# Performance work log

Measured on AMD Instinct MI355X. Metric: run time of the kernel, lower is better.

## Reference

```python
import jax, jax.numpy as jnp
import numpy as np
import math

B, T, D = 4, 8192, 1024
EPS = 1e-5

def setup_inputs() -> dict:
    key = jax.random.key(0)
    ks = jax.random.split(key, 8)
    xavier = lambda k, shape: jax.random.uniform(k, shape, jnp.float32,
                                                 -math.sqrt(6.0 / (shape[0] + shape[1])),
                                                 math.sqrt(6.0 / (shape[0] + shape[1])))
    x = jax.random.normal(ks[0], (B, T, D), jnp.float32)
    ln_gamma = jnp.ones((D,), jnp.float32)
    ln_beta = jnp.zeros((D,), jnp.float32)
    Wg = xavier(ks[1], (D, D))            # torch Linear weight: (out, in)
    bg = jnp.zeros((D,), jnp.float32)
    Wv = 0.01 * xavier(ks[2], (D, D))     # gain=0.01
    bv = jnp.zeros((D,), jnp.float32)
    Wo = 0.01 * xavier(ks[3], (D, D))     # gain=0.01
    bo = jnp.zeros((D,), jnp.float32)
    log_decay = jnp.asarray(math.log(math.exp(0.01) - 1.0), jnp.float32)
    return {"x": x, "ln_gamma": ln_gamma, "ln_beta": ln_beta,
            "Wg": Wg, "bg": bg, "Wv": Wv, "bv": bv, "Wo": Wo, "bo": bo,
            "log_decay": log_decay}

def reference(x, ln_gamma, ln_beta, Wg, bg, Wv, bv, Wo, bo, log_decay):
    # LayerNorm
    mu = jnp.mean(x, axis=-1, keepdims=True)
    var = jnp.mean(jnp.square(x - mu), axis=-1, keepdims=True)
    normed = (x - mu) * jax.lax.rsqrt(var + EPS) * ln_gamma + ln_beta
    # gate / value projections (torch Linear: y = x @ W.T + b)
    g = jax.nn.sigmoid(jnp.einsum('btd,ed->bte', normed, Wg) + bg)
    v = jnp.einsum('btd,ed->bte', normed, Wv) + bv
    # push-pull cumulative sums over time
    cumsum = jnp.cumsum(g * v, axis=1) - jnp.cumsum((1.0 - g) * v, axis=1)
    # positional exponential decay
    alpha = jax.nn.softplus(log_decay)
    positions = jnp.arange(x.shape[1], dtype=jnp.float32)
    decay = jnp.exp(-alpha * positions)[None, :, None]  # (1,T,1)
    out = jnp.einsum('btd,ed->bte', cumsum * decay, Wo) + bo
    return x + out  # dropout is identity at eval
```

## Files before the change

kernel.cpp:

```cpp
#include <hip/hip_runtime.h>
#include <cstdint>
#include <cstddef>

#define DD 1024
#define TT 8192
#define BB 4
#define MM (BB*TT)
#define NCHUNK 64
#define CLEN 128
#define EPS 1e-5f
#define NIT 8

typedef __attribute__((ext_vector_type(8))) short bf16x8;
typedef __attribute__((ext_vector_type(4))) float f32x4;

__device__ __forceinline__ float bf2f(unsigned short b) {
  union { unsigned int u; float f; } c; c.u = ((unsigned int)b) << 16; return c.f;
}
__device__ __forceinline__ unsigned short f2bf(float f) {
  union { float f; unsigned int u; } c; c.f = f;
  unsigned int lsb = (c.u >> 16) & 1u;
  c.u += 0x7fffu + lsb;
  return (unsigned short)(c.u >> 16);
}

__device__ __forceinline__ void gload16(const void* gsrc, void* ldst) {
  __builtin_amdgcn_global_load_lds(
      (const __attribute__((address_space(1))) unsigned int*)gsrc,
      (__attribute__((address_space(3))) unsigned int*)ldst, 16, 0, 0);
}

#define MFMA16(a, b, c) __builtin_amdgcn_mfma_f32_16x16x32_bf16((a), (b), (c), 0, 0, 0)
#define BAR    __builtin_amdgcn_s_barrier()
#define PRIO1  __builtin_amdgcn_s_setprio(1)
#define PRIO0  __builtin_amdgcn_s_setprio(0)
#define VMW(N) asm volatile("s_waitcnt vmcnt(" #N ")" ::: "memory")

__device__ __forceinline__ bf16x8 LD(const char* p, int imm) {
  return *(const bf16x8*)(p + imm);
}

__global__ __launch_bounds__(256) void cast_weights(
    const float* __restrict__ wg, const float* __restrict__ wv,
    const float* __restrict__ wo,
    unsigned short* __restrict__ owg, unsigned short* __restrict__ owv,
    unsigned short* __restrict__ owo) {
  int i = blockIdx.x * 256 + threadIdx.x;
  const float* src; unsigned short* dst; int off;
  if (i < 262144)       { src = wg; dst = owg; off = i; }
  else if (i < 524288)  { src = wv; dst = owv; off = i - 262144; }
  else                  { src = wo; dst = owo; off = i - 524288; }
  float4 v = ((const float4*)src)[off];
  ushort4 o;
  o.x = f2bf(v.x); o.y = f2bf(v.y); o.z = f2bf(v.z); o.w = f2bf(v.w);
  ((ushort4*)dst)[off] = o;
}

__global__ __launch_bounds__(256) void ln_kernel(
    const float* __restrict__ x, const float* __restrict__ gamma,
    const float* __restrict__ beta, unsigned short* __restrict__ normed) {
  size_t row = blockIdx.x;
  int tid = threadIdx.x, lane = tid & 63, wid = tid >> 6;
  float4 v = ((const float4*)(x + row * DD))[tid];
  float s = v.x + v.y + v.z + v.w;
  float q = v.x * v.x + v.y * v.y + v.z * v.z + v.w * v.w;
#pragma unroll
  for (int off = 32; off; off >>= 1) {
    s += __shfl_down(s, off);
    q += __shfl_down(q, off);
  }
  __shared__ float rs[4], rq[4];
  if (lane == 0) { rs[wid] = s; rq[wid] = q; }
  __syncthreads();
  float ts = rs[0] + rs[1] + rs[2] + rs[3];
  float tq = rq[0] + rq[1] + rq[2] + rq[3];
  float mu  = ts * (1.0f / DD);
  float var = tq * (1.0f / DD) - mu * mu;
  float rstd = rsqrtf(var + EPS);
  float4 gm = ((const float4*)gamma)[tid];
  float4 bt = ((const float4*)beta)[tid];
  ushort4 o;
  o.x = f2bf((v.x - mu) * rstd * gm.x + bt.x);
  o.y = f2bf((v.y - mu) * rstd * gm.y + bt.y);
  o.z = f2bf((v.z - mu) * rstd * gm.z + bt.z);
  o.w = f2bf((v.w - mu) * rstd * gm.w + bt.w);
  ((ushort4*)normed)[row * (DD / 4) + tid] = o;
}

__global__ __launch_bounds__(512, 2) void gemm_gv(
    const unsigned short* __restrict__ normed,
    const unsigned short* __restrict__ wg, const unsigned short* __restrict__ wv,
    const float* __restrict__ bg, const float* __restrict__ bv,
    unsigned short* __restrict__ u, float* __restrict__ sums) {
  __shared__ unsigned short As[2][2][128 * 64];
  __shared__ unsigned short Bgs[2][128 * 64];
  __shared__ unsigned short Bvs[2][128 * 64];
  int tid = threadIdx.x, lane = tid & 63, wid = tid >> 6;
  int wm = wid >> 2, wn = wid & 3;
  int swz = (blockIdx.x & 7) * (gridDim.x >> 3) + (blockIdx.x >> 3);
  int bx = swz >> 3, by = swz & 7;
  size_t m0 = (size_t)bx * 256;
  int n0 = by * 128;

  int ua = tid, ub = tid + 512;
  int ra = ua >> 3, sa = (ua & 7) ^ (ra & 7);
  int rb = ub >> 3, sb = (ub & 7) ^ (rb & 7);
  const unsigned short* gA = normed + m0 * DD;
  const unsigned short* gBg = wg + (size_t)n0 * DD;
  const unsigned short* gBv = wv + (size_t)n0 * DD;
  const unsigned short* pAa = gA + (size_t)ra * DD + sa * 8;
  const unsigned short* pAb = gA + (size_t)rb * DD + sb * 8;
  const unsigned short* pGa = gBg + (size_t)ra * DD + sa * 8;
  const unsigned short* pGb = gBg + (size_t)rb * DD + sb * 8;
  const unsigned short* pVa = gBv + (size_t)ra * DD + sa * 8;
  const unsigned short* pVb = gBv + (size_t)rb * DD + sb * 8;
  auto SA = [&](int t, int h) {
    char* d = (char*)&As[t & 1][h][0];
    gload16(pAa + (size_t)h * 128 * DD + t * 64, d + ua * 16);
    gload16(pAb + (size_t)h * 128 * DD + t * 64, d + ub * 16);
  };
  auto SG = [&](int t) {
    char* d = (char*)&Bgs[t & 1][0];
    gload16(pGa + t * 64, d + ua * 16);
    gload16(pGb + t * 64, d + ub * 16);
  };
  auto SV = [&](int t) {
    char* d = (char*)&Bvs[t & 1][0];
    gload16(pVa + t * 64, d + ua * 16);
    gload16(pVb + t * 64, d + ub * 16);
  };

  f32x4 accg[8][2], accv[8][2];
#pragma unroll
  for (int a = 0; a < 8; ++a)
#pragma unroll
    for (int b = 0; b < 2; ++b) {
      accg[a][b] = (f32x4){0.f, 0.f, 0.f, 0.f};
      accv[a][b] = (f32x4){0.f, 0.f, 0.f, 0.f};
    }

  SG(0); SV(0); SA(0, 0); SA(0, 1); SG(1); SV(1); SA(1, 0);
  VMW(6);
  BAR;

  int r = lane & 15, q = lane >> 4, rx = r & 7;
  const char* pA[2][2];
  const char* pBgL[2][2];
  const char* pBvL[2][2];
#pragma unroll
  for (int d = 0; d < 2; ++d) {
#pragma unroll
    for (int kk = 0; kk < 2; ++kk) {
      int s8 = kk * 4 + q;
      int xo = (s8 ^ rx) << 4;
      pA[d][kk]   = (const char*)&As[d][wm][0] + r * 128 + xo;
      pBgL[d][kk] = (const char*)&Bgs[d][0] + (wn * 32 + r) * 128 + xo;
      pBvL[d][kk] = (const char*)&Bvs[d][0] + (wn * 32 + r) * 128 + xo;
    }
  }

  bf16x8 am[4][2], bgf[2][2], bvf[2][2];
  for (int T = 0; T < NIT; ++T) {
    bool more = (T < NIT - 1);
    int t1 = 2 * T + 1, t2 = 2 * T + 2, t3 = 2 * T + 3;
#pragma unroll
    for (int mi = 0; mi < 4; ++mi)
#pragma unroll
      for (int kk = 0; kk < 2; ++kk)
        am[mi][kk] = LD(pA[0][kk], mi * 2048);
#pragma unroll
    for (int ni = 0; ni < 2; ++ni)
#pragma unroll
      for (int kk = 0; kk < 2; ++kk)
        bgf[ni][kk] = LD(pBgL[0][kk], ni * 2048);
    SA(t1, 1);
    BAR; PRIO1;
#pragma unroll
    for (int mi = 0; mi < 4; ++mi)
#pragma unroll
      for (int ni = 0; ni < 2; ++ni)
#pragma unroll
        for (int kk = 0; kk < 2; ++kk)
          accg[mi][ni] = MFMA16(am[mi][kk], bgf[ni][kk], accg[mi][ni]);
    PRIO0; BAR;
#pragma unroll
    for (int ni = 0; ni < 2; ++ni)
#pragma unroll
      for (int kk = 0; kk < 2; ++kk)
        bvf[ni][kk] = LD(pBvL[0][kk], ni * 2048);
    if (more) SG(t2);
    BAR; PRIO1;
#pragma unroll
    for (int mi = 0; mi < 4; ++mi)
#pragma unroll
      for (int ni = 0; ni < 2; ++ni)
#pragma unroll
        for (int kk = 0; kk < 2; ++kk)
          accv[mi][ni] = MFMA16(am[mi][kk], bvf[ni][kk], accv[mi][ni]);
    PRIO0; BAR;
#pragma unroll
    for (int mi = 0; mi < 4; ++mi)
#pragma unroll
      for (int kk = 0; kk < 2; ++kk)
        am[mi][kk] = LD(pA[0][kk], 8192 + mi * 2048);
    if (more) SV(t2);
    BAR; PRIO1;
#pragma unroll
    for (int mi = 0; mi < 4; ++mi)
#pragma unroll
      for (int ni = 0; ni < 2; ++ni)
#pragma unroll
        for (int kk = 0; kk < 2; ++kk)
          accv[4 + mi][ni] = MFMA16(am[mi][kk], bvf[ni][kk], accv[4 + mi][ni]);
    PRIO0; BAR;
    if (more) { SA(t2, 0); VMW(6); } else { VMW(0); }
    BAR; PRIO1;
#pragma unroll
    for (int mi = 0; mi < 4; ++mi)
#pragma unroll
      for (int ni = 0; ni < 2; ++ni)
#pragma unroll
        for (int kk = 0; kk < 2; ++kk)
          accg[4 + mi][ni] = MFMA16(am[mi][kk], bgf[ni][kk], accg[4 + mi][ni]);
    PRIO0; BAR;
#pragma unroll
    for (int mi = 0; mi < 4; ++mi)
#pragma unroll
      for (int kk = 0; kk < 2; ++kk)
        am[mi][kk] = LD(pA[1][kk], mi * 2048);
#pragma unroll
    for (int ni = 0; ni < 2; ++ni)
#pragma unroll
      for (int kk = 0; kk < 2; ++kk)
        bgf[ni][kk] = LD(pBgL[1][kk], ni * 2048);
    if (more) SA(t2, 1);
    BAR; PRIO1;
#pragma unroll
    for (int mi = 0; mi < 4; ++mi)
#pragma unroll
      for (int ni = 0; ni < 2; ++ni)
#pragma unroll
        for (int kk = 0; kk < 2; ++kk)
          accg[mi][ni] = MFMA16(am[mi][kk], bgf[ni][kk], accg[mi][ni]);
    PRIO0; BAR;
#pragma unroll
    for (int ni = 0; ni < 2; ++ni)
#pragma unroll
      for (int kk = 0; kk < 2; ++kk)
        bvf[ni][kk] = LD(pBvL[1][kk], ni * 2048);
    if (more) SG(t3);
    BAR; PRIO1;
#pragma unroll
    for (int mi = 0; mi < 4; ++mi)
#pragma unroll
      for (int ni = 0; ni < 2; ++ni)
#pragma unroll
        for (int kk = 0; kk < 2; ++kk)
          accv[mi][ni] = MFMA16(am[mi][kk], bvf[ni][kk], accv[mi][ni]);
    PRIO0; BAR;
#pragma unroll
    for (int mi = 0; mi < 4; ++mi)
#pragma unroll
      for (int kk = 0; kk < 2; ++kk)
        am[mi][kk] = LD(pA[1][kk], 8192 + mi * 2048);
    if (more) SV(t3);
    BAR; PRIO1;
#pragma unroll
    for (int mi = 0; mi < 4; ++mi)
#pragma unroll
      for (int ni = 0; ni < 2; ++ni)
#pragma unroll
        for (int kk = 0; kk < 2; ++kk)
          accv[4 + mi][ni] = MFMA16(am[mi][kk], bvf[ni][kk], accv[4 + mi][ni]);
    PRIO0; BAR;
    if (more) { SA(t3, 0); VMW(6); } else { VMW(0); }
    BAR; PRIO1;
#pragma unroll
    for (int mi = 0; mi < 4; ++mi)
#pragma unroll
      for (int ni = 0; ni < 2; ++ni)
#pragma unroll
        for (int kk = 0; kk < 2; ++kk)
          accg[4 + mi][ni] = MFMA16(am[mi][kk], bgf[ni][kk], accg[4 + mi][ni]);
    PRIO0; BAR;
  }

  float psum[2] = {0.f, 0.f};
#pragma unroll
  for (int mi = 0; mi < 8; ++mi)
#pragma unroll
    for (int ni = 0; ni < 2; ++ni) {
      int e = n0 + wn * 32 + ni * 16 + r;
      size_t rbase = m0 + wm * 128 + mi * 16 + q * 4;
      float bgv = bg[e], bvv = bv[e];
#pragma unroll
      for (int j = 0; j < 4; ++j) {
        float gp = accg[mi][ni][j] + bgv;
        float vp = accv[mi][ni][j] + bvv;
        float sg = 1.0f / (1.0f + __expf(-gp));
        float uu = (2.0f * sg - 1.0f) * vp;
        psum[ni] += uu;
        u[(rbase + j) * DD + e] = f2bf(uu);
      }
    }
#pragma unroll
  for (int ni = 0; ni < 2; ++ni) {
    psum[ni] += __shfl_xor(psum[ni], 16);
    psum[ni] += __shfl_xor(psum[ni], 32);
  }
  if (lane < 16) {
    int b = (int)(m0 >> 13);
    int ch = (int)((m0 & 8191) >> 7) + wm;
    size_t sidx = ((size_t)(b * NCHUNK + ch)) * DD + n0 + wn * 32 + lane;
    sums[sidx]      = psum[0];
    sums[sidx + 16] = psum[1];
  }
}

__global__ __launch_bounds__(256) void scan_chunks(float* __restrict__ sums) {
  int b = blockIdx.x >> 2;
  int e = (blockIdx.x & 3) * 256 + threadIdx.x;
  float vals[NCHUNK];
#pragma unroll
  for (int c = 0; c < NCHUNK; ++c)
    vals[c] = sums[((size_t)(b * NCHUNK + c)) * DD + e];
  float carry = 0.f;
#pragma unroll
  for (int c = 0; c < NCHUNK; ++c) {
    float t = vals[c]; vals[c] = carry; carry += t;
  }
#pragma unroll
  for (int c = 0; c < NCHUNK; ++c)
    sums[((size_t)(b * NCHUNK + c)) * DD + e] = vals[c];
}

__global__ __launch_bounds__(128) void scan_final(
    unsigned short* __restrict__ u, const float* __restrict__ sums,
    const float* __restrict__ log_decay) {
  int bid = blockIdx.x;
  int half = bid & 1, chunk = (bid >> 1) & 63, b = bid >> 7;
  int e0 = half * 512 + threadIdx.x * 4;
  float alpha = log1pf(__expf(log_decay[0]));
  float dec  = __expf(-alpha * (float)(chunk * CLEN));
  float step = __expf(-alpha);
  float4 c = *(const float4*)(sums + ((size_t)(b * NCHUNK + chunk)) * DD + e0);
  size_t base = ((size_t)b * TT + (size_t)chunk * CLEN) * DD + e0;
#pragma unroll 4
  for (int i = 0; i < CLEN; ++i) {
    ushort4 w = *(const ushort4*)(u + base + (size_t)i * DD);
    c.x += bf2f(w.x); c.y += bf2f(w.y); c.z += bf2f(w.z); c.w += bf2f(w.w);
    ushort4 o;
    o.x = f2bf(c.x * dec); o.y = f2bf(c.y * dec);
    o.z = f2bf(c.z * dec); o.w = f2bf(c.w * dec);
    *(ushort4*)(u + base + (size_t)i * DD) = o;
    dec *= step;
  }
}

__global__ __launch_bounds__(512, 2) void gemm_out(
    const unsigned short* __restrict__ cmat, const unsigned short* __restrict__ wo,
    const float* __restrict__ bo, const float* __restrict__ x,
    float* __restrict__ out) {
  __shared__ unsigned short As[2][2][128 * 64];
  __shared__ unsigned short Bs[2][2][128 * 64];
  int tid = threadIdx.x, lane = tid & 63, wid = tid >> 6;
  int wm = wid >> 2, wn = wid & 3;
  int swz = (blockIdx.x & 7) * (gridDim.x >> 3) + (blockIdx.x >> 3);
  int bx = swz >> 2, by = swz & 3;
  size_t m0 = (size_t)bx * 256;
  int n0 = by * 256;
  int bh = wn >> 1, nb = wn & 1;

  int ua = tid, ub = tid + 512;
  int ra = ua >> 3, sa = (ua & 7) ^ (ra & 7);
  int rb = ub >> 3, sb = (ub & 7) ^ (rb & 7);
  const unsigned short* gA = cmat + m0 * DD;
  const unsigned short* gB = wo + (size_t)n0 * DD;
  const unsigned short* pAa = gA + (size_t)ra * DD + sa * 8;
  const unsigned short* pAb = gA + (size_t)rb * DD + sb * 8;
  const unsigned short* pBa = gB + (size_t)ra * DD + sa * 8;
  const unsigned short* pBb = gB + (size_t)rb * DD + sb * 8;
  auto SA = [&](int t, int h) {
    char* d = (char*)&As[t & 1][h][0];
    gload16(pAa + (size_t)h * 128 * DD + t * 64, d + ua * 16);
    gload16(pAb + (size_t)h * 128 * DD + t * 64, d + ub * 16);
  };
  auto SB = [&](int t, int h) {
    char* d = (char*)&Bs[t & 1][h][0];
    gload16(pBa + (size_t)h * 128 * DD + t * 64, d + ua * 16);
    gload16(pBb + (size_t)h * 128 * DD + t * 64, d + ub * 16);
  };

  f32x4 acc[8][4];
#pragma unroll
  for (int a = 0; a < 8; ++a)
#pragma unroll
    for (int b = 0; b < 4; ++b) acc[a][b] = (f32x4){0.f, 0.f, 0.f, 0.f};

  SB(0, 0); SB(0, 1); SA(0, 0); SA(0, 1); SB(1, 0); SB(1, 1);
  VMW(4);
  BAR;

  int r = lane & 15, q = lane >> 4, rx = r & 7;
  const char* pA[2][2];
  const char* pB[2][2];
#pragma unroll
  for (int d = 0; d < 2; ++d) {
#pragma unroll
    for (int kk = 0; kk < 2; ++kk) {
      int s8 = kk * 4 + q;
      int xo = (s8 ^ rx) << 4;
      pA[d][kk] = (const char*)&As[d][wm][0] + r * 128 + xo;
      pB[d][kk] = (const char*)&Bs[d][bh][0] + (nb * 64 + r) * 128 + xo;
    }
  }

  bf16x8 am[4][2], b01[2][2], b23[2][2];
  for (int T = 0; T < NIT; ++T) {
    bool more = (T < NIT - 1);
    int t1 = 2 * T + 1, t2 = 2 * T + 2, t3 = 2 * T + 3;
#pragma unroll
    for (int mi = 0; mi < 4; ++mi)
#pragma unroll
      for (int kk = 0; kk < 2; ++kk)
        am[mi][kk] = LD(pA[0][kk], mi * 2048);
#pragma unroll
    for (int ni = 0; ni < 2; ++ni)
#pragma unroll
      for (int kk = 0; kk < 2; ++kk)
        b01[ni][kk] = LD(pB[0][kk], ni * 2048);
    SA(t1, 0);
    BAR; PRIO1;
#pragma unroll
    for (int mi = 0; mi < 4; ++mi)
#pragma unroll
      for (int ni = 0; ni < 2; ++ni)
#pragma unroll
        for (int kk = 0; kk < 2; ++kk)
          acc[mi][ni] = MFMA16(am[mi][kk], b01[ni][kk], acc[mi][ni]);
    PRIO0; BAR;
#pragma unroll
    for (int ni = 0; ni < 2; ++ni)
#pragma unroll
      for (int kk = 0; kk < 2; ++kk)
        b23[ni][kk] = LD(pB[0][kk], 4096 + ni * 2048);
    SA(t1, 1);
    BAR; PRIO1;
#pragma unroll
    for (int mi = 0; mi < 4; ++mi)
#pragma unroll
      for (int ni = 0; ni < 2; ++ni)
#pragma unroll
        for (int kk = 0; kk < 2; ++kk)
          acc[mi][2 + ni] = MFMA16(am[mi][kk], b23[ni][kk], acc[mi][2 + ni]);
    PRIO0; BAR;
#pragma unroll
    for (int mi = 0; mi < 4; ++mi)
#pragma unroll
      for (int kk = 0; kk < 2; ++kk)
        am[mi][kk] = LD(pA[0][kk], 8192 + mi * 2048);
    if (more) SB(t2, 0);
    BAR; PRIO1;
#pragma unroll
    for (int mi = 0; mi < 4; ++mi)
#pragma unroll
      for (int ni = 0; ni < 2; ++ni)
#pragma unroll
        for (int kk = 0; kk < 2; ++kk)
          acc[4 + mi][2 + ni] = MFMA16(am[mi][kk], b23[ni][kk], acc[4 + mi][2 + ni]);
    PRIO0; BAR;
    if (more) { SB(t2, 1); VMW(4); } else { VMW(0); }
    BAR; PRIO1;
#pragma unroll
    for (int mi = 0; mi < 4; ++mi)
#pragma unroll
      for (int ni = 0; ni < 2; ++ni)
#pragma unroll
        for (int kk = 0; kk < 2; ++kk)
          acc[4 + mi][ni] = MFMA16(am[mi][kk], b01[ni][kk], acc[4 + mi][ni]);
    PRIO0; BAR;
#pragma unroll
    for (int mi = 0; mi < 4; ++mi)
#pragma unroll
      for (int kk = 0; kk < 2; ++kk)
        am[mi][kk] = LD(pA[1][kk], mi * 2048);
#pragma unroll
    for (int ni = 0; ni < 2; ++ni)
#pragma unroll
      for (int kk = 0; kk < 2; ++kk)
        b01[ni][kk] = LD(pB[1][kk], ni * 2048);
    if (more) SA(t2, 0);
    BAR; PRIO1;
#pragma unroll
    for (int mi = 0; mi < 4; ++mi)
#pragma unroll
      for (int ni = 0; ni < 2; ++ni)
#pragma unroll
        for (int kk = 0; kk < 2; ++kk)
          acc[mi][ni] = MFMA16(am[mi][kk], b01[ni][kk], acc[mi][ni]);
    PRIO0; BAR;
#pragma unroll
    for (int ni = 0; ni < 2; ++ni)
#pragma unroll
      for (int kk = 0; kk < 2; ++kk)
        b23[ni][kk] = LD(pB[1][kk], 4096 + ni * 2048);
    if (more) SA(t2, 1);
    BAR; PRIO1;
#pragma unroll
    for (int mi = 0; mi < 4; ++mi)
#pragma unroll
      for (int ni = 0; ni < 2; ++ni)
#pragma unroll
        for (int kk = 0; kk < 2; ++kk)
          acc[mi][2 + ni] = MFMA16(am[mi][kk], b23[ni][kk], acc[mi][2 + ni]);
    PRIO0; BAR;
#pragma unroll
    for (int mi = 0; mi < 4; ++mi)
#pragma unroll
      for (int kk = 0; kk < 2; ++kk)
        am[mi][kk] = LD(pA[1][kk], 8192 + mi * 2048);
    if (more) SB(t3, 0);
    BAR; PRIO1;
#pragma unroll
    for (int mi = 0; mi < 4; ++mi)
#pragma unroll
      for (int ni = 0; ni < 2; ++ni)
#pragma unroll
        for (int kk = 0; kk < 2; ++kk)
          acc[4 + mi][2 + ni] = MFMA16(am[mi][kk], b23[ni][kk], acc[4 + mi][2 + ni]);
    PRIO0; BAR;
    if (more) { SB(t3, 1); VMW(4); } else { VMW(0); }
    BAR; PRIO1;
#pragma unroll
    for (int mi = 0; mi < 4; ++mi)
#pragma unroll
      for (int ni = 0; ni < 2; ++ni)
#pragma unroll
        for (int kk = 0; kk < 2; ++kk)
          acc[4 + mi][ni] = MFMA16(am[mi][kk], b01[ni][kk], acc[4 + mi][ni]);
    PRIO0; BAR;
  }

#pragma unroll
  for (int mi = 0; mi < 8; ++mi)
#pragma unroll
    for (int nq = 0; nq < 4; ++nq) {
      int e = n0 + wn * 64 + nq * 16 + r;
      size_t rbase = m0 + wm * 128 + mi * 16 + q * 4;
      float bov = bo[e];
#pragma unroll
      for (int j = 0; j < 4; ++j) {
        size_t idx = (rbase + j) * DD + e;
        out[idx] = x[idx] + bov + acc[mi][nq][j];
      }
    }
}

extern "C" void kernel_launch(void* const* d_in, const int* in_sizes, int n_in,
                              void* d_out, int out_size, void* d_ws, size_t ws_size,
                              hipStream_t stream) {
  const float* x     = (const float*)d_in[0];
  const float* gamma = (const float*)d_in[1];
  const float* beta  = (const float*)d_in[2];
  const float* Wg    = (const float*)d_in[3];
  const float* bg    = (const float*)d_in[4];
  const float* Wv    = (const float*)d_in[5];
  const float* bv    = (const float*)d_in[6];
  const float* Wo    = (const float*)d_in[7];
  const float* bo    = (const float*)d_in[8];
  const float* ldcy  = (const float*)d_in[9];
  float* out = (float*)d_out;

  char* ws = (char*)d_ws;
  unsigned short* normed = (unsigned short*)ws;
  unsigned short* u      = (unsigned short*)(ws + (size_t)67108864);
  unsigned short* wgb    = (unsigned short*)(ws + (size_t)134217728);
  unsigned short* wvb    = wgb + 1048576;
  unsigned short* wob    = wvb + 1048576;
  float* sums            = (float*)(ws + (size_t)134217728 + (size_t)3 * 2097152);

  cast_weights<<<3072, 256, 0, stream>>>(Wg, Wv, Wo, wgb, wvb, wob);
  ln_kernel<<<MM, 256, 0, stream>>>(x, gamma, beta, normed);
  gemm_gv<<<dim3(MM / 256 * (DD / 128)), 512, 0, stream>>>(normed, wgb, wvb, bg, bv, u, sums);
  scan_chunks<<<BB * (DD / 256), 256, 0, stream>>>(sums);
  scan_final<<<BB * NCHUNK * 2, 128, 0, stream>>>(u, sums, ldcy);
  gemm_out<<<dim3(MM / 256 * (DD / 256)), 512, 0, stream>>>(u, wob, bo, x, out);
}
```

Before: 335.9 us.

## Interleave gate and value weights into one concatenated matrix for single GEMM

Weight casting now writes Wg and Wv rows interleaved (alternating per row) into one 2048-row bf16 matrix, so the gate/value projection runs as a single 256x256-tile GEMM over a unified B buffer rather than two separate B streams. The epilogue pairs adjacent columns with a lane shuffle to combine gate and value before computing the push-pull product and chunk sums. This simplifies the staged pipeline and uniformly loads B tiles, at the cost of half the lanes idling in the epilogue and extra shuffles.

After: 398.7 us. 1.19x slower.

```diff
diff --git a/kernel.cpp b/kernel.cpp
--- a/kernel.cpp
+++ b/kernel.cpp
@@ -43,17 +43,16 @@
 __global__ __launch_bounds__(256) void cast_weights(
     const float* __restrict__ wg, const float* __restrict__ wv,
     const float* __restrict__ wo,
-    unsigned short* __restrict__ owg, unsigned short* __restrict__ owv,
-    unsigned short* __restrict__ owo) {
+    unsigned short* __restrict__ wcat, unsigned short* __restrict__ owo) {
   int i = blockIdx.x * 256 + threadIdx.x;
-  const float* src; unsigned short* dst; int off;
-  if (i < 262144)       { src = wg; dst = owg; off = i; }
-  else if (i < 524288)  { src = wv; dst = owv; off = i - 262144; }
-  else                  { src = wo; dst = owo; off = i - 524288; }
+  const float* src; unsigned short* dst; int off, dun;
+  if (i < 262144)       { src = wg; off = i;          dst = wcat; dun = ((off & ~255) << 1) | (off & 255); }
+  else if (i < 524288)  { src = wv; off = i - 262144; dst = wcat; dun = ((off & ~255) << 1) | 256 | (off & 255); }
+  else                  { src = wo; off = i - 524288; dst = owo;  dun = off; }
   float4 v = ((const float4*)src)[off];
   ushort4 o;
   o.x = f2bf(v.x); o.y = f2bf(v.y); o.z = f2bf(v.z); o.w = f2bf(v.w);
-  ((ushort4*)dst)[off] = o;
+  ((ushort4*)dst)[dun] = o;
 }
 
 __global__ __launch_bounds__(256) void ln_kernel(
@@ -89,77 +88,64 @@
 
 __global__ __launch_bounds__(512, 2) void gemm_gv(
     const unsigned short* __restrict__ normed,
-    const unsigned short* __restrict__ wg, const unsigned short* __restrict__ wv,
+    const unsigned short* __restrict__ wcat,
     const float* __restrict__ bg, const float* __restrict__ bv,
     unsigned short* __restrict__ u, float* __restrict__ sums) {
   __shared__ unsigned short As[2][2][128 * 64];
-  __shared__ unsigned short Bgs[2][128 * 64];
-  __shared__ unsigned short Bvs[2][128 * 64];
+  __shared__ unsigned short Bs[2][2][128 * 64];
   int tid = threadIdx.x, lane = tid & 63, wid = tid >> 6;
   int wm = wid >> 2, wn = wid & 3;
   int swz = (blockIdx.x & 7) * (gridDim.x >> 3) + (blockIdx.x >> 3);
   int bx = swz >> 3, by = swz & 7;
   size_t m0 = (size_t)bx * 256;
-  int n0 = by * 128;
+  int n0 = by * 256;
+  int bh = wn >> 1, nb = wn & 1;
 
   int ua = tid, ub = tid + 512;
   int ra = ua >> 3, sa = (ua & 7) ^ (ra & 7);
   int rb = ub >> 3, sb = (ub & 7) ^ (rb & 7);
   const unsigned short* gA = normed + m0 * DD;
-  const unsigned short* gBg = wg + (size_t)n0 * DD;
-  const unsigned short* gBv = wv + (size_t)n0 * DD;
+  const unsigned short* gB = wcat + (size_t)n0 * DD;
   const unsigned short* pAa = gA + (size_t)ra * DD + sa * 8;
   const unsigned short* pAb = gA + (size_t)rb * DD + sb * 8;
-  const unsigned short* pGa = gBg + (size_t)ra * DD + sa * 8;
-  const unsigned short* pGb = gBg + (size_t)rb * DD + sb * 8;
-  const unsigned short* pVa = gBv + (size_t)ra * DD + sa * 8;
-  const unsigned short* pVb = gBv + (size_t)rb * DD + sb * 8;
+  const unsigned short* pBa = gB + (size_t)ra * DD + sa * 8;
+  const unsigned short* pBb = gB + (size_t)rb * DD + sb * 8;
   auto SA = [&](int t, int h) {
     char* d = (char*)&As[t & 1][h][0];
     gload16(pAa + (size_t)h * 128 * DD + t * 64, d + ua * 16);
     gload16(pAb + (size_t)h * 128 * DD + t * 64, d + ub * 16);
   };
-  auto SG = [&](int t) {
-    char* d = (char*)&Bgs[t & 1][0];
-    gload16(pGa + t * 64, d + ua * 16);
-    gload16(pGb + t * 64, d + ub * 16);
+  auto SB = [&](int t, int h) {
+    char* d = (char*)&Bs[t & 1][h][0];
+    gload16(pBa + (size_t)h * 128 * DD + t * 64, d + ua * 16);
+    gload16(pBb + (size_t)h * 128 * DD + t * 64, d + ub * 16);
   };
-  auto SV = [&](int t) {
-    char* d = (char*)&Bvs[t & 1][0];
-    gload16(pVa + t * 64, d + ua * 16);
-    gload16(pVb + t * 64, d + ub * 16);
-  };
-
-  f32x4 accg[8][2], accv[8][2];
+
+  f32x4 acc[8][4];
 #pragma unroll
   for (int a = 0; a < 8; ++a)
 #pragma unroll
-    for (int b = 0; b < 2; ++b) {
-      accg[a][b] = (f32x4){0.f, 0.f, 0.f, 0.f};
-      accv[a][b] = (f32x4){0.f, 0.f, 0.f, 0.f};
-    }
-
-  SG(0); SV(0); SA(0, 0); SA(0, 1); SG(1); SV(1); SA(1, 0);
-  VMW(6);
+    for (int b = 0; b < 4; ++b) acc[a][b] = (f32x4){0.f, 0.f, 0.f, 0.f};
+
+  SB(0, 0); SB(0, 1); SA(0, 0); SA(0, 1); SB(1, 0); SB(1, 1);
+  VMW(4);
   BAR;
 
   int r = lane & 15, q = lane >> 4, rx = r & 7;
   const char* pA[2][2];
-  const char* pBgL[2][2];
-  const char* pBvL[2][2];
+  const char* pB[2][2];
 #pragma unroll
   for (int d = 0; d < 2; ++d) {
 #pragma unroll
     for (int kk = 0; kk < 2; ++kk) {
       int s8 = kk * 4 + q;
       int xo = (s8 ^ rx) << 4;
-      pA[d][kk]   = (const char*)&As[d][wm][0] + r * 128 + xo;
-      pBgL[d][kk] = (const char*)&Bgs[d][0] + (wn * 32 + r) * 128 + xo;
-      pBvL[d][kk] = (const char*)&Bvs[d][0] + (wn * 32 + r) * 128 + xo;
+      pA[d][kk] = (const char*)&As[d][wm][0] + r * 128 + xo;
+      pB[d][kk] = (const char*)&Bs[d][bh][0] + (nb * 64 + r) * 128 + xo;
     }
   }
 
-  bf16x8 am[4][2], bgf[2][2], bvf[2][2];
+  bf16x8 am[4][2], b01[2][2], b23[2][2];
   for (int T = 0; T < NIT; ++T) {
     bool more = (T < NIT - 1);
     int t1 = 2 * T + 1, t2 = 2 * T + 2, t3 = 2 * T + 3;
@@ -172,7 +158,22 @@
     for (int ni = 0; ni < 2; ++ni)
 #pragma unroll
       for (int kk = 0; kk < 2; ++kk)
-        bgf[ni][kk] = LD(pBgL[0][kk], ni * 2048);
+        b01[ni][kk] = LD(pB[0][kk], ni * 2048);
+    SA(t1, 0);
+    BAR; PRIO1;
+#pragma unroll
+    for (int mi = 0; mi < 4; ++mi)
+#pragma unroll
+      for (int ni = 0; ni < 2; ++ni)
+#pragma unroll
+        for (int kk = 0; kk < 2; ++kk)
+          acc[mi][ni] = MFMA16(am[mi][kk], b01[ni][kk], acc[mi][ni]);
+    PRIO0; BAR;
+#pragma unroll
+    for (int ni = 0; ni < 2; ++ni)
+#pragma unroll
+      for (int kk = 0; kk < 2; ++kk)
+        b23[ni][kk] = LD(pB[0][kk], 4096 + ni * 2048);
     SA(t1, 1);
     BAR; PRIO1;
 #pragma unroll
@@ -181,47 +182,32 @@
       for (int ni = 0; ni < 2; ++ni)
 #pragma unroll
         for (int kk = 0; kk < 2; ++kk)
-          accg[mi][ni] = MFMA16(am[mi][kk], bgf[ni][kk], accg[mi][ni]);
-    PRIO0; BAR;
-#pragma unroll
-    for (int ni = 0; ni < 2; ++ni)
-#pragma unroll
-      for (int kk = 0; kk < 2; ++kk)
-        bvf[ni][kk] = LD(pBvL[0][kk], ni * 2048);
-    if (more) SG(t2);
-    BAR; PRIO1;
-#pragma unroll
-    for (int mi = 0; mi < 4; ++mi)
-#pragma unroll
-      for (int ni = 0; ni < 2; ++ni)
-#pragma unroll
-        for (int kk = 0; kk < 2; ++kk)
-          accv[mi][ni] = MFMA16(am[mi][kk], bvf[ni][kk], accv[mi][ni]);
+          acc[mi][2 + ni] = MFMA16(am[mi][kk], b23[ni][kk], acc[mi][2 + ni]);
     PRIO0; BAR;
 #pragma unroll
     for (int mi = 0; mi < 4; ++mi)
 #pragma unroll
       for (int kk = 0; kk < 2; ++kk)
         am[mi][kk] = LD(pA[0][kk], 8192 + mi * 2048);
-    if (more) SV(t2);
-    BAR; PRIO1;
-#pragma unroll
-    for (int mi = 0; mi < 4; ++mi)
-#pragma unroll
-      for (int ni = 0; ni < 2; ++ni)
-#pragma unroll
-        for (int kk = 0; kk < 2; ++kk)
-          accv[4 + mi][ni] = MFMA16(am[mi][kk], bvf[ni][kk], accv[4 + mi][ni]);
-    PRIO0; BAR;
-    if (more) { SA(t2, 0); VMW(6); } else { VMW(0); }
-    BAR; PRIO1;
-#pragma unroll
-    for (int mi = 0; mi < 4; ++mi)
-#pragma unroll
-      for (int ni = 0; ni < 2; ++ni)
-#pragma unroll
-        for (int kk = 0; kk < 2; ++kk)
-          accg[4 + mi][ni] = MFMA16(am[mi][kk], bgf[ni][kk], accg[4 + mi][ni]);
+    if (more) SB(t2, 0);
+    BAR; PRIO1;
+#pragma unroll
+    for (int mi = 0; mi < 4; ++mi)
+#pragma unroll
+      for (int ni = 0; ni < 2; ++ni)
+#pragma unroll
+        for (int kk = 0; kk < 2; ++kk)
+          acc[4 + mi][2 + ni] = MFMA16(am[mi][kk], b23[ni][kk], acc[4 + mi][2 + ni]);
+    PRIO0; BAR;
+    if (more) { SB(t2, 1); VMW(4); } else { VMW(0); }
+    BAR; PRIO1;
+#pragma unroll
+    for (int mi = 0; mi < 4; ++mi)
+#pragma unroll
+      for (int ni = 0; ni < 2; ++ni)
+#pragma unroll
+        for (int kk = 0; kk < 2; ++kk)
+          acc[4 + mi][ni] = MFMA16(am[mi][kk], b01[ni][kk], acc[4 + mi][ni]);
     PRIO0; BAR;
 #pragma unroll
     for (int mi = 0; mi < 4; ++mi)
@@ -232,7 +218,22 @@
     for (int ni = 0; ni < 2; ++ni)
 #pragma unroll
       for (int kk = 0; kk < 2; ++kk)
-        bgf[ni][kk] = LD(pBgL[1][kk], ni * 2048);
+        b01[ni][kk] = LD(pB[1][kk], ni * 2048);
+    if (more) SA(t2, 0);
+    BAR; PRIO1;
+#pragma unroll
+    for (int mi = 0; mi < 4; ++mi)
+#pragma unroll
+      for (int ni = 0; ni < 2; ++ni)
+#pragma unroll
+        for (int kk = 0; kk < 2; ++kk)
+          acc[mi][ni] = MFMA16(am[mi][kk], b01[ni][kk], acc[mi][ni]);
+    PRIO0; BAR;
+#pragma unroll
+    for (int ni = 0; ni < 2; ++ni)
+#pragma unroll
+      for (int kk = 0; kk < 2; ++kk)
+        b23[ni][kk] = LD(pB[1][kk], 4096 + ni * 2048);
     if (more) SA(t2, 1);
     BAR; PRIO1;
 #pragma unroll
@@ -241,79 +242,71 @@
       for (int ni = 0; ni < 2; ++ni)
 #pragma unroll
         for (int kk = 0; kk < 2; ++kk)
-          accg[mi][ni] = MFMA16(am[mi][kk], bgf[ni][kk], accg[mi][ni]);
-    PRIO0; BAR;
-#pragma unroll
-    for (int ni = 0; ni < 2; ++ni)
-#pragma unroll
-      for (int kk = 0; kk < 2; ++kk)
-        bvf[ni][kk] = LD(pBvL[1][kk], ni * 2048);
-    if (more) SG(t3);
-    BAR; PRIO1;
-#pragma unroll
-    for (int mi = 0; mi < 4; ++mi)
-#pragma unroll
-      for (int ni = 0; ni < 2; ++ni)
-#pragma unroll
-        for (int kk = 0; kk < 2; ++kk)
-          accv[mi][ni] = MFMA16(am[mi][kk], bvf[ni][kk], accv[mi][ni]);
+          acc[mi][2 + ni] = MFMA16(am[mi][kk], b23[ni][kk], acc[mi][2 + ni]);
     PRIO0; BAR;
 #pragma unroll
     for (int mi = 0; mi < 4; ++mi)
 #pragma unroll
       for (int kk = 0; kk < 2; ++kk)
         am[mi][kk] = LD(pA[1][kk], 8192 + mi * 2048);
-    if (more) SV(t3);
-    BAR; PRIO1;
-#pragma unroll
-    for (int mi = 0; mi < 4; ++mi)
-#pragma unroll
-      for (int ni = 0; ni < 2; ++ni)
-#pragma unroll
-        for (int kk = 0; kk < 2; ++kk)
-          accv[4 + mi][ni] = MFMA16(am[mi][kk], bvf[ni][kk], accv[4 + mi][ni]);
-    PRIO0; BAR;
-    if (more) { SA(t3, 0); VMW(6); } else { VMW(0); }
-    BAR; PRIO1;
-#pragma unroll
-    for (int mi = 0; mi < 4; ++mi)
-#pragma unroll
-      for (int ni = 0; ni < 2; ++ni)
-#pragma unroll
-        for (int kk = 0; kk < 2; ++kk)
-          accg[4 + mi][ni] = MFMA16(am[mi][kk], bgf[ni][kk], accg[4 + mi][ni]);
-    PRIO0; BAR;
-  }
-
-  float psum[2] = {0.f, 0.f};
-#pragma unroll
-  for (int mi = 0; mi < 8; ++mi)
-#pragma unroll
-    for (int ni = 0; ni < 2; ++ni) {
-      int e = n0 + wn * 32 + ni * 16 + r;
-      size_t rbase = m0 + wm * 128 + mi * 16 + q * 4;
-      float bgv = bg[e], bvv = bv[e];
+    if (more) SB(t3, 0);
+    BAR; PRIO1;
+#pragma unroll
+    for (int mi = 0; mi < 4; ++mi)
+#pragma unroll
+      for (int ni = 0; ni < 2; ++ni)
+#pragma unroll
+        for (int kk = 0; kk < 2; ++kk)
+          acc[4 + mi][2 + ni] = MFMA16(am[mi][kk], b23[ni][kk], acc[4 + mi][2 + ni]);
+    PRIO0; BAR;
+    if (more) { SB(t3, 1); VMW(4); } else { VMW(0); }
+    BAR; PRIO1;
+#pragma unroll
+    for (int mi = 0; mi < 4; ++mi)
+#pragma unroll
+      for (int ni = 0; ni < 2; ++ni)
+#pragma unroll
+        for (int kk = 0; kk < 2; ++kk)
+          acc[4 + mi][ni] = MFMA16(am[mi][kk], b01[ni][kk], acc[4 + mi][ni]);
+    PRIO0; BAR;
+  }
+
+  float psum[4] = {0.f, 0.f, 0.f, 0.f};
+  int ebase = (n0 + bh * 128 + nb * 64) >> 1;
+  bool even = (r & 1) == 0;
+#pragma unroll
+  for (int nq = 0; nq < 4; ++nq) {
+    int e = ebase + nq * 8 + (r >> 1);
+    float bgv = bg[e], bvv = bv[e];
+#pragma unroll
+    for (int mi = 0; mi < 8; ++mi) {
+      size_t row = m0 + wm * 128 + mi * 16 + q * 4;
 #pragma unroll
       for (int j = 0; j < 4; ++j) {
-        float gp = accg[mi][ni][j] + bgv;
-        float vp = accv[mi][ni][j] + bvv;
-        float sg = 1.0f / (1.0f + __expf(-gp));
-        float uu = (2.0f * sg - 1.0f) * vp;
-        psum[ni] += uu;
-        u[(rbase + j) * DD + e] = f2bf(uu);
+        float self = acc[mi][nq][j];
+        float other = __shfl_xor(self, 1);
+        if (even) {
+          float gp = self + bgv;
+          float vp = other + bvv;
+          float sg = 1.0f / (1.0f + __expf(-gp));
+          float uu = (2.0f * sg - 1.0f) * vp;
+          psum[nq] += uu;
+          u[(row + j) * DD + e] = f2bf(uu);
+        }
       }
     }
-#pragma unroll
-  for (int ni = 0; ni < 2; ++ni) {
-    psum[ni] += __shfl_xor(psum[ni], 16);
-    psum[ni] += __shfl_xor(psum[ni], 32);
-  }
-  if (lane < 16) {
+  }
+#pragma unroll
+  for (int nq = 0; nq < 4; ++nq) {
+    psum[nq] += __shfl_xor(psum[nq], 16);
+    psum[nq] += __shfl_xor(psum[nq], 32);
+  }
+  if (even && q == 0) {
     int b = (int)(m0 >> 13);
     int ch = (int)((m0 & 8191) >> 7) + wm;
-    size_t sidx = ((size_t)(b * NCHUNK + ch)) * DD + n0 + wn * 32 + lane;
-    sums[sidx]      = psum[0];
-    sums[sidx + 16] = psum[1];
+    size_t sb0 = ((size_t)(b * NCHUNK + ch)) * DD + ebase + (r >> 1);
+#pragma unroll
+    for (int nq = 0; nq < 4; ++nq) sums[sb0 + nq * 8] = psum[nq];
   }
 }
 
@@ -574,14 +567,13 @@
   char* ws = (char*)d_ws;
   unsigned short* normed = (unsigned short*)ws;
   unsigned short* u      = (unsigned short*)(ws + (size_t)67108864);
-  unsigned short* wgb    = (unsigned short*)(ws + (size_t)134217728);
-  unsigned short* wvb    = wgb + 1048576;
-  unsigned short* wob    = wvb + 1048576;
-  float* sums            = (float*)(ws + (size_t)134217728 + (size_t)3 * 2097152);
-
-  cast_weights<<<3072, 256, 0, stream>>>(Wg, Wv, Wo, wgb, wvb, wob);
+  unsigned short* wcat   = (unsigned short*)(ws + (size_t)134217728);
+  unsigned short* wob    = wcat + 2097152;
+  float* sums            = (float*)(ws + (size_t)134217728 + (size_t)6291456);
+
+  cast_weights<<<3072, 256, 0, stream>>>(Wg, Wv, Wo, wcat, wob);
   ln_kernel<<<MM, 256, 0, stream>>>(x, gamma, beta, normed);
-  gemm_gv<<<dim3(MM / 256 * (DD / 128)), 512, 0, stream>>>(normed, wgb, wvb, bg, bv, u, sums);
+  gemm_gv<<<dim3(MM / 256 * 8), 512, 0, stream>>>(normed, wcat, bg, bv, u, sums);
   scan_chunks<<<BB * (DD / 256), 256, 0, stream>>>(sums);
   scan_final<<<BB * NCHUNK * 2, 128, 0, stream>>>(u, sums, ldcy);
   gemm_out<<<dim3(MM / 256 * (DD / 256)), 512, 0, stream>>>(u, wob, bo, x, out);
```
